# Performance work log

Measured on AMD Instinct MI355X. Metric: run time of the kernel, lower is better.

The kernel has to match this reference:

```python
import jax, jax.numpy as jnp
import numpy as np

B, T, S, D = 8, 16, 256, 1024
H, KVH, HD = 16, 4, 64
GROUPS = H // KVH
SCALE = HD ** -0.5
CAP = 50.0
EPS = 1e-6


def setup_inputs() -> dict:
    key = jax.random.key(0)
    ks = jax.random.split(key, 5)
    return {
        "x": jax.random.normal(ks[0], (B, T, S, D), dtype=jnp.float32),
        "Wq": jax.random.normal(ks[1], (D, H * HD), dtype=jnp.float32) * (D ** -0.5),
        "Wk": jax.random.normal(ks[2], (D, KVH * HD), dtype=jnp.float32) * (D ** -0.5),
        "Wv": jax.random.normal(ks[3], (D, KVH * HD), dtype=jnp.float32) * (D ** -0.5),
        "Wo": jax.random.normal(ks[4], (H * HD, D), dtype=jnp.float32) * ((H * HD) ** -0.5),
        "q_norm_w": jnp.ones((HD,), dtype=jnp.float32),
        "k_norm_w": jnp.ones((HD,), dtype=jnp.float32),
    }


def _rmsnorm(x, w):
    rms = jnp.sqrt(jnp.mean(x * x, axis=-1, keepdims=True) + EPS)
    return x / rms * w


def reference(x, Wq, Wk, Wv, Wo, q_norm_w, k_norm_w):
    b, t, s, d = x.shape
    xf = x.reshape(b * t, s, d)                    # (BT, S, D)
    q = (xf @ Wq).reshape(b * t, s, H, HD).transpose(0, 2, 1, 3)   # (BT, H, S, hd)
    k = (xf @ Wk).reshape(b * t, s, KVH, HD).transpose(0, 2, 1, 3)  # (BT, KVH, S, hd)
    v = (xf @ Wv).reshape(b * t, s, KVH, HD).transpose(0, 2, 1, 3)
    q = _rmsnorm(q, q_norm_w)
    k = _rmsnorm(k, k_norm_w)
    if GROUPS > 1:
        k = jnp.repeat(k, GROUPS, axis=1)          # (BT, H, S, hd)
        v = jnp.repeat(v, GROUPS, axis=1)
    logits = jnp.einsum("bhqd,bhkd->bhqk", q, k) * SCALE
    logits = CAP * jnp.tanh(logits / CAP)          # soft cap
    attn = jax.nn.softmax(logits, axis=-1)
    out = jnp.einsum("bhqk,bhkd->bhqd", attn, v)   # (BT, H, S, hd)
    out = out.transpose(0, 2, 1, 3).reshape(b * t, s, H * HD)
    out = out @ Wo
    return out.reshape(b, t, s, d)
```

## Files before the change

kernel.cpp:

```cpp
#include <hip/hip_runtime.h>
#include <cstdint>
#include <cstddef>

typedef __bf16 bf16x8 __attribute__((ext_vector_type(8)));
typedef float f32x4 __attribute__((ext_vector_type(4)));
typedef unsigned short u16;
typedef unsigned int u32;
typedef unsigned short u16x8 __attribute__((ext_vector_type(8)));

#define ROWS 32768
#define DMODEL 1024
#define NQKV 1536
#define C1_ 0.0072134752044448170f
#define A2_ 144.26950408889634f
#define B2_ 72.13475204444817f

__device__ __forceinline__ u16 f2bf(float f) {
    unsigned u = __float_as_uint(f);
    u += 0x7fffu + ((u >> 16) & 1u);
    return (u16)(u >> 16);
}
__device__ __forceinline__ float bf_lo(u32 u) { return __uint_as_float(u << 16); }
__device__ __forceinline__ float bf_hi(u32 u) { return __uint_as_float(u & 0xffff0000u); }
__device__ __forceinline__ u32 pack_rne(float lo, float hi) {
    return (u32)f2bf(lo) | ((u32)f2bf(hi) << 16);
}

__global__ __launch_bounds__(256) void f32_to_bf16_vec(
    const float* __restrict__ in, u16* __restrict__ out, int n4)
{
    int i = blockIdx.x * 256 + threadIdx.x;
    if (i >= n4) return;
    float4 f = ((const float4*)in)[i];
    ushort4 u;
    u.x = f2bf(f.x); u.y = f2bf(f.y); u.z = f2bf(f.z); u.w = f2bf(f.w);
    ((ushort4*)out)[i] = u;
}

__global__ __launch_bounds__(256) void transpose_bf16(
    const float* __restrict__ src, u16* __restrict__ dst, int R, int C)
{
    __shared__ float tile[32][33];
    int c0 = blockIdx.x * 32;
    int r0 = blockIdx.y * 32;
    int tx = threadIdx.x & 31;
    int ty = threadIdx.x >> 5;
#pragma unroll
    for (int i = 0; i < 32; i += 8)
        tile[ty + i][tx] = src[(size_t)(r0 + ty + i) * C + (c0 + tx)];
    __syncthreads();
#pragma unroll
    for (int i = 0; i < 32; i += 8)
        dst[(size_t)(c0 + ty + i) * R + (r0 + tx)] = f2bf(tile[tx][ty + i]);
}

template<bool BF16OUT, int NY, bool AHB>
__global__ __launch_bounds__(256) void gemm_bt(
    const u16* __restrict__ A, const u16* __restrict__ Bt,
    void* __restrict__ Cout, int M, int N, int K)
{
    __shared__ u16 As[128][32];
    __shared__ u16 Bs[128][32];
    const int tid  = threadIdx.x;
    const int wave = tid >> 6;
    const int lane = tid & 63;
    const int q4   = lane >> 4;
    const int cl   = lane & 15;
    const int wr   = wave >> 1, wc = wave & 1;
    const int id   = blockIdx.y * gridDim.x + blockIdx.x;
    const int cpx  = (gridDim.x * gridDim.y) >> 3;
    const int swz  = (id & 7) * cpx + (id >> 3);
    const int m0   = (swz / NY) * 128;
    const int n0   = (swz % NY) * 128;
    const int srow = lane >> 2;
    const int skoff = (lane & 3) * 8;

    const f32x4 zero = {0.f, 0.f, 0.f, 0.f};
    f32x4 acc[4][4];
#pragma unroll
    for (int i = 0; i < 4; ++i)
#pragma unroll
        for (int j = 0; j < 4; ++j) acc[i][j] = zero;

    for (int k0 = 0; k0 < K; k0 += 32) {
        __syncthreads();
#pragma unroll
        for (int cc = 0; cc < 2; ++cc) {
            int r = 32 * wave + 16 * cc + srow;
            const u16* ga;
            if (AHB) {
                int hh = k0 >> 6;
                ga = A + ((size_t)hh * M + (m0 + r)) * 64 + (k0 & 63) + skoff;
            } else {
                ga = A + (size_t)(m0 + r) * K + k0 + skoff;
            }
            __builtin_amdgcn_global_load_lds(
                (const __attribute__((address_space(1))) void*)ga,
                (__attribute__((address_space(3))) void*)(&As[32 * wave + 16 * cc][0]),
                16, 0, 0);
            const u16* gb = Bt + (size_t)(n0 + r) * K + k0 + skoff;
            __builtin_amdgcn_global_load_lds(
                (const __attribute__((address_space(1))) void*)gb,
                (__attribute__((address_space(3))) void*)(&Bs[32 * wave + 16 * cc][0]),
                16, 0, 0);
        }
        __syncthreads();
        bf16x8 af[4], bfr[4];
#pragma unroll
        for (int i = 0; i < 4; ++i)
            af[i] = *(const bf16x8*)&As[64 * wr + 16 * i + cl][q4 * 8];
#pragma unroll
        for (int j = 0; j < 4; ++j)
            bfr[j] = *(const bf16x8*)&Bs[64 * wc + 16 * j + cl][q4 * 8];
#pragma unroll
        for (int i = 0; i < 4; ++i)
#pragma unroll
            for (int j = 0; j < 4; ++j)
                acc[i][j] = __builtin_amdgcn_mfma_f32_16x16x32_bf16(
                    af[i], bfr[j], acc[i][j], 0, 0, 0);
    }

#pragma unroll
    for (int i = 0; i < 4; ++i)
#pragma unroll
        for (int j = 0; j < 4; ++j)
#pragma unroll
            for (int r = 0; r < 4; ++r) {
                int row = m0 + 64 * wr + 16 * i + q4 * 4 + r;
                int col = n0 + 64 * wc + 16 * j + cl;
                if (BF16OUT)
                    ((u16*)Cout)[(size_t)row * N + col] = f2bf(acc[i][j][r]);
                else
                    ((float*)Cout)[(size_t)row * N + col] = acc[i][j][r];
            }
}

__global__ __launch_bounds__(256, 3) void attention_kernel(
    const u16* __restrict__ qkv, const float* __restrict__ qw,
    const float* __restrict__ kw, u16* __restrict__ ao)
{
    const int lg  = (blockIdx.x & 7) * 256 + (blockIdx.x >> 3);
    const int bt  = lg >> 4;
    const int h   = lg & 15;
    const int kvh = h >> 2;
    const int tid  = threadIdx.x;
    const int wave = tid >> 6;
    const int lane = tid & 63;
    const int q4   = lane >> 4;
    const int cl   = lane & 15;

    __shared__ __align__(16) u16 Vt[64][264];
    __shared__ __align__(16) u16 P[4][64][40];

    {
        const u16* vrow = qkv + (size_t)(bt * 256 + tid) * NQKV + 1280 + kvh * 64;
#pragma unroll
        for (int ch = 0; ch < 8; ++ch) {
            u16x8 v8 = *(const u16x8*)(vrow + ch * 8);
#pragma unroll
            for (int e = 0; e < 8; ++e) Vt[ch * 8 + e][tid] = v8[e];
        }
    }
    __syncthreads();

    const u16* qbase = qkv + (size_t)(bt * 256) * NQKV + h * 64;
    const u16* kbase = qkv + (size_t)(bt * 256) * NQKV + 1024 + kvh * 64;

    uint4 qa[2][4];
    float rq[4];
    float wqk[2][8];
#pragma unroll
    for (int ks = 0; ks < 2; ++ks)
#pragma unroll
        for (int e = 0; e < 8; ++e) {
            int d = ks * 32 + q4 * 8 + e;
            wqk[ks][e] = qw[d] * kw[d];
        }
#pragma unroll
    for (int i = 0; i < 4; ++i) {
#pragma unroll
        for (int ks = 0; ks < 2; ++ks)
            qa[ks][i] = *(const uint4*)(qbase +
                (size_t)(wave * 64 + 16 * i + cl) * NQKV + ks * 32 + q4 * 8);
        float ss = 0.f;
#pragma unroll
        for (int ks = 0; ks < 2; ++ks) {
            const u32* u = (const u32*)&qa[ks][i];
#pragma unroll
            for (int e = 0; e < 4; ++e) {
                float lo = bf_lo(u[e]), hi = bf_hi(u[e]);
                ss += lo * lo + hi * hi;
            }
        }
        ss += __shfl_xor(ss, 16, 64);
        ss += __shfl_xor(ss, 32, 64);
        rq[i] = rsqrtf(ss * (1.0f / 64.0f) + 1e-6f);
#pragma unroll
        for (int ks = 0; ks < 2; ++ks) {
            u32* u = (u32*)&qa[ks][i];
#pragma unroll
            for (int e = 0; e < 4; ++e) {
                float lo = bf_lo(u[e]) * wqk[ks][2 * e];
                float hi = bf_hi(u[e]) * wqk[ks][2 * e + 1];
                u[e] = pack_rne(lo, hi);
            }
        }
    }
    float rqc[4][4];
#pragma unroll
    for (int i = 0; i < 4; ++i)
#pragma unroll
        for (int r = 0; r < 4; ++r)
            rqc[i][r] = __shfl(rq[i], 4 * q4 + r, 64);

    const f32x4 zero = {0.f, 0.f, 0.f, 0.f};
    f32x4 o[4][4];
    f32x4 lacc[4];
#pragma unroll
    for (int i = 0; i < 4; ++i) {
        lacc[i] = zero;
#pragma unroll
        for (int j = 0; j < 4; ++j) o[i][j] = zero;
    }
    bf16x8 ones;
#pragma unroll
    for (int e = 0; e < 8; ++e) ones[e] = (__bf16)1.0f;

    for (int nb = 0; nb < 4; ++nb) {
#pragma unroll
        for (int jh = 0; jh < 2; ++jh) {
#pragma unroll
            for (int jj = 0; jj < 2; ++jj) {
                const int j = 2 * jh + jj;
                uint4 kb[2];
#pragma unroll
                for (int ks = 0; ks < 2; ++ks)
                    kb[ks] = *(const uint4*)(kbase +
                        (size_t)(nb * 64 + 16 * j + cl) * NQKV + ks * 32 + q4 * 8);
                float ss = 0.f;
#pragma unroll
                for (int ks = 0; ks < 2; ++ks) {
                    const u32* u = (const u32*)&kb[ks];
#pragma unroll
                    for (int e = 0; e < 4; ++e) {
                        float lo = bf_lo(u[e]), hi = bf_hi(u[e]);
                        ss += lo * lo + hi * hi;
                    }
                }
                ss += __shfl_xor(ss, 16, 64);
                ss += __shfl_xor(ss, 32, 64);
                float rkc1 = rsqrtf(ss * (1.0f / 64.0f) + 1e-6f) * C1_;

#pragma unroll
                for (int i = 0; i < 4; ++i) {
                    f32x4 s = __builtin_amdgcn_mfma_f32_16x16x32_bf16(
                        *(const bf16x8*)&qa[0][i], *(const bf16x8*)&kb[0], zero, 0, 0, 0);
                    s = __builtin_amdgcn_mfma_f32_16x16x32_bf16(
                        *(const bf16x8*)&qa[1][i], *(const bf16x8*)&kb[1], s, 0, 0, 0);
#pragma unroll
                    for (int r = 0; r < 4; ++r) {
                        float e2 = __builtin_amdgcn_exp2f(s[r] * rqc[i][r] * rkc1);
                        float rc = __builtin_amdgcn_rcpf(e2 + 1.0f);
                        float p  = __builtin_amdgcn_exp2f(fmaf(-A2_, rc, B2_));
                        P[wave][16 * i + q4 * 4 + r][16 * jj + cl] = f2bf(p);
                    }
                }
            }
            bf16x8 vb[4];
#pragma unroll
            for (int j2 = 0; j2 < 4; ++j2)
                vb[j2] = *(const bf16x8*)&Vt[16 * j2 + cl][nb * 64 + jh * 32 + q4 * 8];
#pragma unroll
            for (int i = 0; i < 4; ++i) {
                bf16x8 pa = *(const bf16x8*)&P[wave][16 * i + cl][q4 * 8];
#pragma unroll
                for (int j2 = 0; j2 < 4; ++j2)
                    o[i][j2] = __builtin_amdgcn_mfma_f32_16x16x32_bf16(
                        pa, vb[j2], o[i][j2], 0, 0, 0);
                lacc[i] = __builtin_amdgcn_mfma_f32_16x16x32_bf16(
                    pa, ones, lacc[i], 0, 0, 0);
            }
        }
    }

    u16* aob = ao + ((size_t)h * ROWS + (size_t)(bt * 256 + wave * 64)) * 64;
#pragma unroll
    for (int i = 0; i < 4; ++i)
#pragma unroll
        for (int r = 0; r < 4; ++r) {
            float inv = 1.0f / lacc[i][r];
            int lr = 16 * i + 4 * q4 + r;
#pragma unroll
            for (int j = 0; j < 4; ++j)
                aob[(size_t)lr * 64 + 16 * j + cl] = f2bf(o[i][j][r] * inv);
        }
}

extern "C" void kernel_launch(void* const* d_in, const int* in_sizes, int n_in,
                              void* d_out, int out_size, void* d_ws, size_t ws_size,
                              hipStream_t stream)
{
    const float* x  = (const float*)d_in[0];
    const float* Wq = (const float*)d_in[1];
    const float* Wk = (const float*)d_in[2];
    const float* Wv = (const float*)d_in[3];
    const float* Wo = (const float*)d_in[4];
    const float* qw = (const float*)d_in[5];
    const float* kw = (const float*)d_in[6];
    float* out = (float*)d_out;

    char* ws = (char*)d_ws;
    u16* Xb  = (u16*)(ws);
    u16* QKV = (u16*)(ws + (size_t)67108864);
    u16* AO  = (u16*)(ws + (size_t)167772160);
    u16* WcT = (u16*)(ws + (size_t)234881024);
    u16* WoT = (u16*)(ws + (size_t)238026752);

    f32_to_bf16_vec<<<dim3(32768), dim3(256), 0, stream>>>(x, Xb, 8388608);
    transpose_bf16<<<dim3(32, 32), dim3(256), 0, stream>>>(Wq, WcT, 1024, 1024);
    transpose_bf16<<<dim3(8, 32), dim3(256), 0, stream>>>(Wk, WcT + (size_t)1024 * 1024, 1024, 256);
    transpose_bf16<<<dim3(8, 32), dim3(256), 0, stream>>>(Wv, WcT + (size_t)1280 * 1024, 1024, 256);
    transpose_bf16<<<dim3(32, 32), dim3(256), 0, stream>>>(Wo, WoT, 1024, 1024);
    gemm_bt<true, 12, false><<<dim3(256, 12), dim3(256), 0, stream>>>(Xb, WcT, (void*)QKV, ROWS, NQKV, 1024);
    attention_kernel<<<dim3(2048), dim3(256), 0, stream>>>(QKV, qw, kw, AO);
    gemm_bt<false, 8, true><<<dim3(256, 8), dim3(256), 0, stream>>>(AO, WoT, (void*)out, ROWS, DMODEL, 1024);
}
```

Before: 656.0 us.

## Keep softmax probabilities in registers via transposed QK^T MFMA layout

Computes S^T = K·Q^T so the MFMA output layout directly matches the A-operand layout for the P·V MFMA. The probabilities are packed to bf16 in registers, which removes the shared-memory P staging buffer. The ones-vector MFMA used for row sums is replaced by scalar accumulation plus a cross-lane reduction. Q/K RMS norms are precomputed once per row in the prologue and kept in shared memory instead of being recomputed with shuffles for every K tile. V is read from LDS in a permuted key order to match, which trades LDS traffic and MFMA work for extra scalar adds and some different LDS access patterns.

```diff
diff --git a/kernel.cpp b/kernel.cpp
--- a/kernel.cpp
+++ b/kernel.cpp
@@ -7,6 +7,7 @@
 typedef unsigned short u16;
 typedef unsigned int u32;
 typedef unsigned short u16x8 __attribute__((ext_vector_type(8)));
+typedef unsigned int u32x4v __attribute__((ext_vector_type(4)));
 
 #define ROWS 32768
 #define DMODEL 1024
@@ -150,24 +151,41 @@
     const int cl   = lane & 15;
 
     __shared__ __align__(16) u16 Vt[64][264];
-    __shared__ __align__(16) u16 P[4][64][40];
+    __shared__ float rk_s[256];
+    __shared__ float rq_s[256];
 
     {
-        const u16* vrow = qkv + (size_t)(bt * 256 + tid) * NQKV + 1280 + kvh * 64;
+        const u16* rowb = qkv + (size_t)(bt * 256 + tid) * NQKV;
+        const u16* vrow = rowb + 1280 + kvh * 64;
 #pragma unroll
         for (int ch = 0; ch < 8; ++ch) {
             u16x8 v8 = *(const u16x8*)(vrow + ch * 8);
 #pragma unroll
             for (int e = 0; e < 8; ++e) Vt[ch * 8 + e][tid] = v8[e];
         }
+        float ssk = 0.f, ssq = 0.f;
+#pragma unroll
+        for (int ch = 0; ch < 8; ++ch) {
+            uint4 kk = *(const uint4*)(rowb + 1024 + kvh * 64 + ch * 8);
+            uint4 qq = *(const uint4*)(rowb + h * 64 + ch * 8);
+            const u32* uk = (const u32*)&kk;
+            const u32* uq = (const u32*)&qq;
+#pragma unroll
+            for (int e = 0; e < 4; ++e) {
+                float lo = bf_lo(uk[e]), hi = bf_hi(uk[e]);
+                ssk += lo * lo + hi * hi;
+                lo = bf_lo(uq[e]); hi = bf_hi(uq[e]);
+                ssq += lo * lo + hi * hi;
+            }
+        }
+        rk_s[tid] = rsqrtf(ssk * (1.0f / 64.0f) + 1e-6f) * C1_;
+        rq_s[tid] = rsqrtf(ssq * (1.0f / 64.0f) + 1e-6f);
     }
     __syncthreads();
 
     const u16* qbase = qkv + (size_t)(bt * 256) * NQKV + h * 64;
     const u16* kbase = qkv + (size_t)(bt * 256) * NQKV + 1024 + kvh * 64;
 
-    uint4 qa[2][4];
-    float rq[4];
     float wqk[2][8];
 #pragma unroll
     for (int ks = 0; ks < 2; ++ks)
@@ -176,27 +194,13 @@
             int d = ks * 32 + q4 * 8 + e;
             wqk[ks][e] = qw[d] * kw[d];
         }
-#pragma unroll
-    for (int i = 0; i < 4; ++i) {
-#pragma unroll
-        for (int ks = 0; ks < 2; ++ks)
+    uint4 qa[2][4];
+#pragma unroll
+    for (int i = 0; i < 4; ++i)
+#pragma unroll
+        for (int ks = 0; ks < 2; ++ks) {
             qa[ks][i] = *(const uint4*)(qbase +
                 (size_t)(wave * 64 + 16 * i + cl) * NQKV + ks * 32 + q4 * 8);
-        float ss = 0.f;
-#pragma unroll
-        for (int ks = 0; ks < 2; ++ks) {
-            const u32* u = (const u32*)&qa[ks][i];
-#pragma unroll
-            for (int e = 0; e < 4; ++e) {
-                float lo = bf_lo(u[e]), hi = bf_hi(u[e]);
-                ss += lo * lo + hi * hi;
-            }
-        }
-        ss += __shfl_xor(ss, 16, 64);
-        ss += __shfl_xor(ss, 32, 64);
-        rq[i] = rsqrtf(ss * (1.0f / 64.0f) + 1e-6f);
-#pragma unroll
-        for (int ks = 0; ks < 2; ++ks) {
             u32* u = (u32*)&qa[ks][i];
 #pragma unroll
             for (int e = 0; e < 4; ++e) {
@@ -205,90 +209,87 @@
                 u[e] = pack_rne(lo, hi);
             }
         }
-    }
-    float rqc[4][4];
-#pragma unroll
-    for (int i = 0; i < 4; ++i)
-#pragma unroll
-        for (int r = 0; r < 4; ++r)
-            rqc[i][r] = __shfl(rq[i], 4 * q4 + r, 64);
+    float rq[4];
+#pragma unroll
+    for (int i = 0; i < 4; ++i)
+        rq[i] = rq_s[wave * 64 + 16 * i + cl];
 
     const f32x4 zero = {0.f, 0.f, 0.f, 0.f};
     f32x4 o[4][4];
-    f32x4 lacc[4];
-#pragma unroll
-    for (int i = 0; i < 4; ++i) {
-        lacc[i] = zero;
+    float lsum[4] = {0.f, 0.f, 0.f, 0.f};
+#pragma unroll
+    for (int i = 0; i < 4; ++i)
 #pragma unroll
         for (int j = 0; j < 4; ++j) o[i][j] = zero;
-    }
-    bf16x8 ones;
-#pragma unroll
-    for (int e = 0; e < 8; ++e) ones[e] = (__bf16)1.0f;
 
     for (int nb = 0; nb < 4; ++nb) {
 #pragma unroll
         for (int jh = 0; jh < 2; ++jh) {
-#pragma unroll
-            for (int jj = 0; jj < 2; ++jj) {
-                const int j = 2 * jh + jj;
-                uint4 kb[2];
+            const int cb = nb * 64 + jh * 32;
+            float rkc[2][4];
+#pragma unroll
+            for (int jj = 0; jj < 2; ++jj)
+#pragma unroll
+                for (int r = 0; r < 4; ++r)
+                    rkc[jj][r] = rk_s[cb + 16 * jj + 4 * q4 + r];
+            uint4 kb[2][2];
+#pragma unroll
+            for (int jj = 0; jj < 2; ++jj)
 #pragma unroll
                 for (int ks = 0; ks < 2; ++ks)
-                    kb[ks] = *(const uint4*)(kbase +
-                        (size_t)(nb * 64 + 16 * j + cl) * NQKV + ks * 32 + q4 * 8);
-                float ss = 0.f;
-#pragma unroll
-                for (int ks = 0; ks < 2; ++ks) {
-                    const u32* u = (const u32*)&kb[ks];
-#pragma unroll
-                    for (int e = 0; e < 4; ++e) {
-                        float lo = bf_lo(u[e]), hi = bf_hi(u[e]);
-                        ss += lo * lo + hi * hi;
-                    }
+                    kb[jj][ks] = *(const uint4*)(kbase +
+                        (size_t)(cb + 16 * jj + cl) * NQKV + ks * 32 + q4 * 8);
+            bf16x8 vb[4];
+#pragma unroll
+            for (int j2 = 0; j2 < 4; ++j2) {
+                uint2 lo4 = *(const uint2*)&Vt[16 * j2 + cl][cb + 4 * q4];
+                uint2 hi4 = *(const uint2*)&Vt[16 * j2 + cl][cb + 16 + 4 * q4];
+                u32x4v vv = {lo4.x, lo4.y, hi4.x, hi4.y};
+                vb[j2] = *(const bf16x8*)&vv;
+            }
+#pragma unroll
+            for (int i = 0; i < 4; ++i) {
+                f32x4 s0 = __builtin_amdgcn_mfma_f32_16x16x32_bf16(
+                    *(const bf16x8*)&kb[0][0], *(const bf16x8*)&qa[0][i], zero, 0, 0, 0);
+                s0 = __builtin_amdgcn_mfma_f32_16x16x32_bf16(
+                    *(const bf16x8*)&kb[0][1], *(const bf16x8*)&qa[1][i], s0, 0, 0, 0);
+                f32x4 s1 = __builtin_amdgcn_mfma_f32_16x16x32_bf16(
+                    *(const bf16x8*)&kb[1][0], *(const bf16x8*)&qa[0][i], zero, 0, 0, 0);
+                s1 = __builtin_amdgcn_mfma_f32_16x16x32_bf16(
+                    *(const bf16x8*)&kb[1][1], *(const bf16x8*)&qa[1][i], s1, 0, 0, 0);
+                float p0[4], p1[4];
+#pragma unroll
+                for (int r = 0; r < 4; ++r) {
+                    float e2a = __builtin_amdgcn_exp2f(s0[r] * rq[i] * rkc[0][r]);
+                    float rca = __builtin_amdgcn_rcpf(e2a + 1.0f);
+                    p0[r] = __builtin_amdgcn_exp2f(fmaf(-A2_, rca, B2_));
+                    float e2b = __builtin_amdgcn_exp2f(s1[r] * rq[i] * rkc[1][r]);
+                    float rcb = __builtin_amdgcn_rcpf(e2b + 1.0f);
+                    p1[r] = __builtin_amdgcn_exp2f(fmaf(-A2_, rcb, B2_));
+                    lsum[i] += p0[r] + p1[r];
                 }
-                ss += __shfl_xor(ss, 16, 64);
-                ss += __shfl_xor(ss, 32, 64);
-                float rkc1 = rsqrtf(ss * (1.0f / 64.0f) + 1e-6f) * C1_;
-
-#pragma unroll
-                for (int i = 0; i < 4; ++i) {
-                    f32x4 s = __builtin_amdgcn_mfma_f32_16x16x32_bf16(
-                        *(const bf16x8*)&qa[0][i], *(const bf16x8*)&kb[0], zero, 0, 0, 0);
-                    s = __builtin_amdgcn_mfma_f32_16x16x32_bf16(
-                        *(const bf16x8*)&qa[1][i], *(const bf16x8*)&kb[1], s, 0, 0, 0);
-#pragma unroll
-                    for (int r = 0; r < 4; ++r) {
-                        float e2 = __builtin_amdgcn_exp2f(s[r] * rqc[i][r] * rkc1);
-                        float rc = __builtin_amdgcn_rcpf(e2 + 1.0f);
-                        float p  = __builtin_amdgcn_exp2f(fmaf(-A2_, rc, B2_));
-                        P[wave][16 * i + q4 * 4 + r][16 * jj + cl] = f2bf(p);
-                    }
-                }
-            }
-            bf16x8 vb[4];
-#pragma unroll
-            for (int j2 = 0; j2 < 4; ++j2)
-                vb[j2] = *(const bf16x8*)&Vt[16 * j2 + cl][nb * 64 + jh * 32 + q4 * 8];
-#pragma unroll
-            for (int i = 0; i < 4; ++i) {
-                bf16x8 pa = *(const bf16x8*)&P[wave][16 * i + cl][q4 * 8];
+                u32x4v paw = {pack_rne(p0[0], p0[1]), pack_rne(p0[2], p0[3]),
+                              pack_rne(p1[0], p1[1]), pack_rne(p1[2], p1[3])};
+                bf16x8 pa = *(const bf16x8*)&paw;
 #pragma unroll
                 for (int j2 = 0; j2 < 4; ++j2)
                     o[i][j2] = __builtin_amdgcn_mfma_f32_16x16x32_bf16(
                         pa, vb[j2], o[i][j2], 0, 0, 0);
-                lacc[i] = __builtin_amdgcn_mfma_f32_16x16x32_bf16(
-                    pa, ones, lacc[i], 0, 0, 0);
             }
         }
     }
 
+#pragma unroll
+    for (int i = 0; i < 4; ++i) {
+        lsum[i] += __shfl_xor(lsum[i], 16, 64);
+        lsum[i] += __shfl_xor(lsum[i], 32, 64);
+    }
     u16* aob = ao + ((size_t)h * ROWS + (size_t)(bt * 256 + wave * 64)) * 64;
 #pragma unroll
     for (int i = 0; i < 4; ++i)
 #pragma unroll
         for (int r = 0; r < 4; ++r) {
-            float inv = 1.0f / lacc[i][r];
+            float inv = 1.0f / __shfl(lsum[i], 4 * q4 + r, 64);
             int lr = 16 * i + 4 * q4 + r;
 #pragma unroll
             for (int j = 0; j < 4; ++j)
```

Measured after the change: 709.5 us. +8.2%, slower.
